# Kernel optimization log

Hardware: AMD Instinct MI355X
Metric: run time of the kernel (lower is better)

Reference implementation:

```python
import jax, jax.numpy as jnp
import numpy as np

NUM_HEADS = 16
HEAD_DIM = 128
WINDOW = 512
ROPE_BASE = 10000.0


def _rope_cos_sin(seq_len):
    inv_freq = 1.0 / (ROPE_BASE ** (jnp.arange(0, HEAD_DIM, 2, dtype=jnp.float32) / HEAD_DIM))
    freqs = jnp.arange(seq_len, dtype=jnp.float32)[:, None] * inv_freq[None, :]  # (s, d/2)
    return jnp.cos(freqs), jnp.sin(freqs)


def _apply_rotary(x, cos, sin):
    # x: (b, h, s, d); cos/sin: (s, d/2). Interleaved pairs as in the torch impl.
    x1, x2 = x[..., ::2], x[..., 1::2]
    c = cos[None, None]
    s = sin[None, None]
    r1 = x1 * c - x2 * s
    r2 = x1 * s + x2 * c
    return jnp.stack([r1, r2], axis=-1).reshape(x.shape)


def setup_inputs() -> dict:
    key = jax.random.key(0)
    ks = jax.random.split(key, 5)
    dim = NUM_HEADS * HEAD_DIM
    x = jax.random.normal(ks[0], (1, 4096, dim), dtype=jnp.float32)
    std = 0.02
    Wq = jax.random.normal(ks[1], (dim, dim), dtype=jnp.float32) * std
    Wk = jax.random.normal(ks[2], (dim, dim), dtype=jnp.float32) * std
    Wv = jax.random.normal(ks[3], (dim, dim), dtype=jnp.float32) * std
    Wo = jax.random.normal(ks[4], (dim, dim), dtype=jnp.float32) * std
    return {"x": x, "Wq": Wq, "Wk": Wk, "Wv": Wv, "Wo": Wo}


def reference(x, Wq, Wk, Wv, Wo):
    b, s, dim = x.shape
    scale = HEAD_DIM ** -0.5

    def split_heads(t):
        return t.reshape(b, s, NUM_HEADS, HEAD_DIM).transpose(0, 2, 1, 3)  # b h s d

    q = split_heads(x @ Wq.T)
    k = split_heads(x @ Wk.T)
    v = split_heads(x @ Wv.T)

    cos, sin = _rope_cos_sin(s)
    q = _apply_rotary(q, cos, sin)
    k = _apply_rotary(k, cos, sin)

    scores = jnp.einsum('bhqd,bhkd->bhqk', q, k) * scale  # (b, h, s, s)
    pos = jnp.arange(s)
    i, j = pos[:, None], pos[None, :]
    mask = (j <= i) & (i - j < WINDOW)  # sliding-window causal
    scores = jnp.where(mask[None, None], scores, -jnp.inf)
    attn = jax.nn.softmax(scores, axis=-1)

    out = jnp.einsum('bhqk,bhkd->bhqd', attn, v)
    out = out.transpose(0, 2, 1, 3).reshape(b, s, dim)
    return out @ Wo.T
```

## Files before the change

### kernel.cpp

```cpp
#include <hip/hip_runtime.h>
#include <hip/hip_bf16.h>
#include <math.h>

#define DIM 2048
#define NH 16
#define HD 128
#define WIN 512

typedef __hip_bfloat16 bf16;
using frag8 = __attribute__((ext_vector_type(8))) short;
using facc4 = __attribute__((ext_vector_type(4))) float;

__device__ inline float toF(const bf16 v) { return __bfloat162float(v); }
template <typename T> __device__ inline T fromF(float v);
template <> __device__ inline float fromF<float>(float v) { return v; }
template <> __device__ inline bf16 fromF<bf16>(float v) { return __float2bfloat16(v); }

__device__ inline unsigned bfb(float x) {
    unsigned u = __float_as_uint(x);
    u += 0x7fffu + ((u >> 16) & 1u);
    return u >> 16;
}

__device__ inline uint4 pack8(const float* p) {
    const float4 v0 = *(const float4*)p;
    const float4 v1 = *(const float4*)(p + 4);
    uint4 r;
    r.x = bfb(v0.x) | (bfb(v0.y) << 16);
    r.y = bfb(v0.z) | (bfb(v0.w) << 16);
    r.z = bfb(v1.x) | (bfb(v1.y) << 16);
    r.w = bfb(v1.z) | (bfb(v1.w) << 16);
    return r;
}

__global__ __launch_bounds__(256) void cvt_f32_bf16(const float* __restrict__ src,
                                                    bf16* __restrict__ dst, int n8) {
    const int i = blockIdx.x * 256 + threadIdx.x;
    if (i < n8) ((uint4*)dst)[i] = pack8(src + (size_t)i * 8);
}

__device__ inline void gload_lds16(const bf16* g, short* l) {
    __builtin_amdgcn_global_load_lds(
        (const __attribute__((address_space(1))) unsigned int*)g,
        (__attribute__((address_space(3))) unsigned int*)l, 16, 0, 0);
}


#define WAIT_LGKM0()                                             \
    do {                                                         \
        asm volatile("s_waitcnt lgkmcnt(0)" ::: "memory");       \
        __builtin_amdgcn_sched_barrier(0);                       \
    } while (0)

#define READ_A(BUF, MI)                                                          \
    do {                                                                         \
        _Pragma("unroll") for (int ii = 0; ii < 4; ++ii)                         \
        _Pragma("unroll") for (int kk = 0; kk < 2; ++kk) {                       \
            const int row_ = wm * 128 + (MI) * 64 + ii * 16 + mr;                \
            const int slot_ = ((kk << 2) + q) ^ (row_ & 7);                      \
            a[ii][kk] = *(const frag8*)&lds[BUF][0][row_][slot_ << 3];           \
        }                                                                        \
    } while (0)

#define READ_B(BUF, NI)                                                          \
    do {                                                                         \
        _Pragma("unroll") for (int jj = 0; jj < 2; ++jj)                         \
        _Pragma("unroll") for (int kk = 0; kk < 2; ++kk) {                       \
            const int row_ = wn * 64 + (NI) * 32 + jj * 16 + mr;                 \
            const int slot_ = ((kk << 2) + q) ^ (row_ & 7);                      \
            b[NI][jj][kk] = *(const frag8*)&lds[BUF][1][row_][slot_ << 3];       \
        }                                                                        \
    } while (0)

#define MFMA_QUAD(MI, NI)                                                        \
    do {                                                                         \
        __builtin_amdgcn_s_setprio(1);                                           \
        _Pragma("unroll") for (int ii = 0; ii < 4; ++ii)                         \
        _Pragma("unroll") for (int jj = 0; jj < 2; ++jj)                         \
        _Pragma("unroll") for (int kk = 0; kk < 2; ++kk)                         \
            acc[(MI) * 4 + ii][(NI) * 2 + jj] =                                  \
                __builtin_amdgcn_mfma_f32_16x16x32_bf16(                         \
                    a[ii][kk], b[NI][jj][kk], acc[(MI) * 4 + ii][(NI) * 2 + jj], \
                    0, 0, 0);                                                    \
        __builtin_amdgcn_s_setprio(0);                                           \
    } while (0)

template <typename TC, bool SPLIT>
__global__ __launch_bounds__(512, 2) void gemm256_8ph(const bf16* __restrict__ A,
                                                      const bf16* __restrict__ B,
                                                      TC* __restrict__ C,
                                                      bf16* __restrict__ Qp,
                                                      bf16* __restrict__ Kp,
                                                      bf16* __restrict__ Vp,
                                                      int M, int N, int K) {
    __shared__ __align__(16) short lds[2][2][256][64];
    const int tid = threadIdx.x;
    const int lane = tid & 63;
    const int w = tid >> 6;

    const int gx = gridDim.x;
    const int nwg = gx * (int)gridDim.y;
    const int lin0 = (int)blockIdx.y * gx + (int)blockIdx.x;
    const int lin = ((nwg & 7) == 0) ? (lin0 & 7) * (nwg >> 3) + (lin0 >> 3) : lin0;
    const int n0 = (lin % gx) * 256;
    const int m0 = (lin / gx) * 256;

    const int wm = w >> 2, wn = w & 3;
    const int q = lane >> 4, mr = lane & 15;
    const int sl = lane & 7, rlo = lane >> 3;
    const int rbA = wm * 128 + wn * 16;
    const int rbB = (w >> 1) * 64 + (w & 1) * 16;

    const int nt = K >> 6;
    const int nIter = nt >> 1;

    facc4 acc[8][4];
#pragma unroll
    for (int i = 0; i < 8; ++i)
#pragma unroll
        for (int j = 0; j < 4; ++j)
#pragma unroll
            for (int r = 0; r < 4; ++r) acc[i][j][r] = 0.f;

    frag8 a[4][2], b[2][2][2];

    auto stage = [&](const bf16* __restrict__ G, int grb, int mat, int buf, int ub, int t) {
        const int kt = t < nt ? t : nt - 1;
        const int k0 = kt << 6;
#pragma unroll
        for (int u = 0; u < 2; ++u) {
            const int row0 = ub + u * 8;
            const int row = row0 + rlo;
            gload_lds16(G + (size_t)(grb + row) * K + k0 + ((sl ^ rlo) << 3),
                        (short*)&lds[buf][mat][row0][0]);
        }
    };

    stage(A, m0, 0, 0, rbA, 0);
    stage(A, m0, 0, 0, rbA + 64, 0);
    stage(B, n0, 1, 0, rbB, 0);
    stage(B, n0, 1, 0, rbB + 32, 0);
    stage(A, m0, 0, 1, rbA, 1);
    stage(B, n0, 1, 1, rbB, 1);
    stage(B, n0, 1, 1, rbB + 32, 1);
    asm volatile("s_waitcnt vmcnt(6)" ::: "memory");
    __builtin_amdgcn_s_barrier();

    for (int it = 0; it < nIter; ++it) {
        const int t2 = 2 * it + 2;
        READ_A(0, 0);
        READ_B(0, 0);
        stage(A, m0, 0, 1, rbA + 64, 2 * it + 1);
        __builtin_amdgcn_s_barrier();
        WAIT_LGKM0();
        MFMA_QUAD(0, 0);
        __builtin_amdgcn_s_barrier();
        READ_B(0, 1);
        stage(A, m0, 0, 0, rbA, t2);
        __builtin_amdgcn_s_barrier();
        WAIT_LGKM0();
        MFMA_QUAD(0, 1);
        __builtin_amdgcn_s_barrier();
        READ_A(0, 1);
        stage(B, n0, 1, 0, rbB, t2);
        __builtin_amdgcn_s_barrier();
        WAIT_LGKM0();
        MFMA_QUAD(1, 0);
        __builtin_amdgcn_s_barrier();
        stage(B, n0, 1, 0, rbB + 32, t2);
        __builtin_amdgcn_s_barrier();
        __builtin_amdgcn_sched_barrier(0);
        MFMA_QUAD(1, 1);
        asm volatile("s_waitcnt vmcnt(6)" ::: "memory");
        __builtin_amdgcn_s_barrier();
        READ_A(1, 0);
        READ_B(1, 0);
        stage(A, m0, 0, 0, rbA + 64, t2);
        __builtin_amdgcn_s_barrier();
        WAIT_LGKM0();
        MFMA_QUAD(0, 0);
        __builtin_amdgcn_s_barrier();
        READ_B(1, 1);
        stage(A, m0, 0, 1, rbA, t2 + 1);
        __builtin_amdgcn_s_barrier();
        WAIT_LGKM0();
        MFMA_QUAD(0, 1);
        __builtin_amdgcn_s_barrier();
        READ_A(1, 1);
        stage(B, n0, 1, 1, rbB, t2 + 1);
        __builtin_amdgcn_s_barrier();
        WAIT_LGKM0();
        MFMA_QUAD(1, 0);
        __builtin_amdgcn_s_barrier();
        stage(B, n0, 1, 1, rbB + 32, t2 + 1);
        __builtin_amdgcn_s_barrier();
        __builtin_amdgcn_sched_barrier(0);
        MFMA_QUAD(1, 1);
        asm volatile("s_waitcnt vmcnt(6)" ::: "memory");
        __builtin_amdgcn_s_barrier();
    }

    if (SPLIT) {
        bf16* dst = (n0 < DIM) ? Qp : ((n0 < 2 * DIM) ? Kp : Vp);
        const int nb = n0 % DIM;
#pragma unroll
        for (int im = 0; im < 8; ++im)
#pragma unroll
            for (int jn = 0; jn < 4; ++jn) {
                const int col = nb + wn * 64 + jn * 16 + mr;
#pragma unroll
                for (int r = 0; r < 4; ++r) {
                    const int row = m0 + wm * 128 + im * 16 + q * 4 + r;
                    dst[(size_t)row * DIM + col] = fromF<bf16>(acc[im][jn][r]);
                }
            }
    } else {
#pragma unroll
        for (int im = 0; im < 8; ++im)
#pragma unroll
            for (int jn = 0; jn < 4; ++jn) {
                const int col = n0 + wn * 64 + jn * 16 + mr;
#pragma unroll
                for (int r = 0; r < 4; ++r) {
                    const int row = m0 + wm * 128 + im * 16 + q * 4 + r;
                    C[(size_t)row * N + col] = fromF<TC>(acc[im][jn][r]);
                }
            }
    }
}

template <typename TC>
__global__ __launch_bounds__(256) void gemm_bt_async(const bf16* __restrict__ A,
                                                     const bf16* __restrict__ B,
                                                     TC* __restrict__ C,
                                                     int M, int N, int K) {
    __shared__ short As[128 * 32];
    __shared__ short Bs[128 * 32];
    const int tid = threadIdx.x;
    const int lane = tid & 63;
    const int w = tid >> 6;
    const int m0 = blockIdx.y * 128;
    const int n0 = blockIdx.x * 128;
    const int wm = (w >> 1) * 64;
    const int wn = (w & 1) * 64;
    const int q = lane >> 4;
    const int mr = lane & 15;

    facc4 acc[4][4];
#pragma unroll
    for (int i = 0; i < 4; ++i)
#pragma unroll
        for (int j = 0; j < 4; ++j)
#pragma unroll
            for (int r = 0; r < 4; ++r) acc[i][j][r] = 0.f;

    for (int k0 = 0; k0 < K; k0 += 32) {
        __syncthreads();
#pragma unroll
        for (int u = 0; u < 2; ++u) {
            const int c = w * 128 + u * 64 + lane;
            const int row = c >> 2, col = (c & 3) * 8;
            gload_lds16(A + (size_t)(m0 + row) * K + k0 + col, As + (w * 128 + u * 64) * 8);
            gload_lds16(B + (size_t)(n0 + row) * K + k0 + col, Bs + (w * 128 + u * 64) * 8);
        }
        __syncthreads();

        frag8 af[4], bfr[4];
#pragma unroll
        for (int i = 0; i < 4; ++i)
            af[i] = *(const frag8*)&As[(wm + 16 * i + mr) * 32 + q * 8];
#pragma unroll
        for (int j = 0; j < 4; ++j)
            bfr[j] = *(const frag8*)&Bs[(wn + 16 * j + mr) * 32 + q * 8];
#pragma unroll
        for (int i = 0; i < 4; ++i)
#pragma unroll
            for (int j = 0; j < 4; ++j)
                acc[i][j] = __builtin_amdgcn_mfma_f32_16x16x32_bf16(af[i], bfr[j], acc[i][j], 0, 0, 0);
    }

#pragma unroll
    for (int i = 0; i < 4; ++i)
#pragma unroll
        for (int j = 0; j < 4; ++j) {
            const int col = n0 + wn + 16 * j + mr;
#pragma unroll
            for (int r = 0; r < 4; ++r) {
                const int row = m0 + wm + 16 * i + q * 4 + r;
                C[(size_t)row * N + col] = fromF<TC>(acc[i][j][r]);
            }
        }
}

__device__ inline uint rot_pair(uint wp, float c, float s) {
    const float x1 = __uint_as_float((wp & 0xFFFFu) << 16);
    const float x2 = __uint_as_float(wp & 0xFFFF0000u);
    const float r1 = x1 * c - x2 * s;
    const float r2 = x1 * s + x2 * c;
    return bfb(r1) | (bfb(r2) << 16);
}

__global__ __launch_bounds__(256) void rope_qk_vec(bf16* __restrict__ Q,
                                                   bf16* __restrict__ K, int S) {
    const int p = blockIdx.x * 256 + threadIdx.x;
    const int per_row = DIM / 8;
    const int s = p / per_row;
    const int off = (p % per_row) * 8;
    const int f0 = (off & 127) >> 1;
    float cs[4], sn[4];
#pragma unroll
    for (int t = 0; t < 4; ++t) {
        const float inv = __expf(-0.14391157f * (float)(f0 + t));
        sincosf((float)s * inv, &sn[t], &cs[t]);
    }
    const size_t base = (size_t)s * DIM + off;
    uint4 qv = *(uint4*)(Q + base);
    qv.x = rot_pair(qv.x, cs[0], sn[0]);
    qv.y = rot_pair(qv.y, cs[1], sn[1]);
    qv.z = rot_pair(qv.z, cs[2], sn[2]);
    qv.w = rot_pair(qv.w, cs[3], sn[3]);
    *(uint4*)(Q + base) = qv;
    uint4 kv = *(uint4*)(K + base);
    kv.x = rot_pair(kv.x, cs[0], sn[0]);
    kv.y = rot_pair(kv.y, cs[1], sn[1]);
    kv.z = rot_pair(kv.z, cs[2], sn[2]);
    kv.w = rot_pair(kv.w, cs[3], sn[3]);
    *(uint4*)(K + base) = kv;
}

__global__ __launch_bounds__(256) void transp_v(const bf16* __restrict__ V,
                                                bf16* __restrict__ Vt, int S) {
    const int tid = threadIdx.x;
    const int lane = tid & 63;
    const int w = tid >> 6;
    const int k0 = blockIdx.x * 64;
    const int h = blockIdx.y;
#pragma unroll
    for (int it = 0; it < 2; ++it) {
        const int kp = lane & 31;
        const int dc = (lane >> 5) + 2 * it + 4 * w;
        const int d0 = dc * 8;
        const bf16* vp = V + (size_t)(k0 + 2 * kp) * DIM + h * HD + d0;
        const uint4 a = *(const uint4*)vp;
        const uint4 b = *(const uint4*)(vp + DIM);
        const uint aw[4] = {a.x, a.y, a.z, a.w};
        const uint bw[4] = {b.x, b.y, b.z, b.w};
#pragma unroll
        for (int e = 0; e < 8; ++e) {
            const uint lo = (aw[e >> 1] >> (16 * (e & 1))) & 0xFFFFu;
            const uint hi = (bw[e >> 1] >> (16 * (e & 1))) & 0xFFFFu;
            ((uint*)Vt)[((((size_t)h * HD + d0 + e) * S + k0) >> 1) + kp] = lo | (hi << 16);
        }
    }
}

__global__ __launch_bounds__(256, 3) void flash_swa(const bf16* __restrict__ Q,
                                                    const bf16* __restrict__ K,
                                                    const bf16* __restrict__ Vt,
                                                    bf16* __restrict__ O, int S) {
    __shared__ __align__(16) char lds[53248];
    short* Qs = (short*)lds;
    short* Ps = (short*)lds;
    short* Ks = (short*)(lds + 17408);
    short* VtL = (short*)(lds + 34816);

    const int tid = threadIdx.x;
    const int lane = tid & 63;
    const int w = tid >> 6;
    const int q = lane >> 4;
    const int mr = lane & 15;
    const int i0 = blockIdx.x * 64;
    const int h = blockIdx.y;
    const float scale = 0.08838834764831845f;

#pragma unroll
    for (int u = 0; u < 4; ++u) {
        const int c = tid + 256 * u;
        const int row = c >> 4, col = (c & 15) * 8;
        *(uint4*)&Qs[row * 136 + col] =
            *(const uint4*)(Q + (size_t)(i0 + row) * DIM + h * HD + col);
    }
    __syncthreads();
    frag8 qf[4];
#pragma unroll
    for (int kk = 0; kk < 4; ++kk)
        qf[kk] = *(const frag8*)&Qs[(w * 16 + mr) * 136 + kk * 32 + q * 8];

    float mrow[4], lrow[4];
    facc4 oacc[8];
#pragma unroll
    for (int r = 0; r < 4; ++r) { mrow[r] = -1e30f; lrow[r] = 0.f; }
#pragma unroll
    for (int dt = 0; dt < 8; ++dt)
#pragma unroll
        for (int r = 0; r < 4; ++r) oacc[dt][r] = 0.f;

    const bf16* vtg = Vt + (size_t)h * HD * S;

    const int t0 = (i0 >= WIN) ? 0 : (WIN - i0) / 64;
    for (int t = t0; t < 9; ++t) {
        const int jb = i0 - WIN + t * 64;
        __syncthreads();

#pragma unroll
        for (int u = 0; u < 4; ++u) {
            const int c = tid + 256 * u;
            const int row = c >> 4, col = (c & 15) * 8;
            *(uint4*)&Ks[row * 136 + col] =
                *(const uint4*)(K + (size_t)(jb + row) * DIM + h * HD + col);
        }
#pragma unroll
        for (int u = 0; u < 4; ++u) {
            const int c = tid + 256 * u;
            const int d = c >> 3, k0c = (c & 7) * 8;
            *(uint4*)&VtL[d * 72 + k0c] = *(const uint4*)(vtg + (size_t)d * S + jb + k0c);
        }
        __syncthreads();

        facc4 sacc[4];
#pragma unroll
        for (int nt = 0; nt < 4; ++nt) {
#pragma unroll
            for (int r = 0; r < 4; ++r) sacc[nt][r] = 0.f;
#pragma unroll
            for (int kk = 0; kk < 4; ++kk) {
                const frag8 kfr = *(const frag8*)&Ks[(nt * 16 + mr) * 136 + kk * 32 + q * 8];
                sacc[nt] = __builtin_amdgcn_mfma_f32_16x16x32_bf16(qf[kk], kfr, sacc[nt], 0, 0, 0);
            }
        }

        float sv[4][4];
        float rmax[4] = {-1e30f, -1e30f, -1e30f, -1e30f};
#pragma unroll
        for (int nt = 0; nt < 4; ++nt) {
            const int j = jb + nt * 16 + mr;
#pragma unroll
            for (int r = 0; r < 4; ++r) {
                const int i = i0 + w * 16 + q * 4 + r;
                const bool valid = (j <= i) && (i - j < WIN);
                sv[nt][r] = valid ? sacc[nt][r] * scale : -1e30f;
                rmax[r] = fmaxf(rmax[r], sv[nt][r]);
            }
        }
#pragma unroll
        for (int msk = 1; msk <= 8; msk <<= 1)
#pragma unroll
            for (int r = 0; r < 4; ++r)
                rmax[r] = fmaxf(rmax[r], __shfl_xor(rmax[r], msk, 64));

        float alpha[4], rsum[4];
#pragma unroll
        for (int r = 0; r < 4; ++r) {
            const float mn = fmaxf(mrow[r], rmax[r]);
            alpha[r] = __expf(mrow[r] - mn);
            mrow[r] = mn;
            rsum[r] = 0.f;
        }
#pragma unroll
        for (int nt = 0; nt < 4; ++nt)
#pragma unroll
            for (int r = 0; r < 4; ++r) {
                const float pv = (sv[nt][r] > -1e29f) ? __expf(sv[nt][r] - mrow[r]) : 0.f;
                rsum[r] += pv;
                Ps[(w * 16 + q * 4 + r) * 72 + nt * 16 + mr] = (short)bfb(pv);
            }
#pragma unroll
        for (int msk = 1; msk <= 8; msk <<= 1)
#pragma unroll
            for (int r = 0; r < 4; ++r)
                rsum[r] += __shfl_xor(rsum[r], msk, 64);
#pragma unroll
        for (int r = 0; r < 4; ++r) lrow[r] = lrow[r] * alpha[r] + rsum[r];
#pragma unroll
        for (int dt = 0; dt < 8; ++dt)
#pragma unroll
            for (int r = 0; r < 4; ++r) oacc[dt][r] *= alpha[r];

        __syncthreads();

#pragma unroll
        for (int ks = 0; ks < 2; ++ks) {
            const frag8 pf = *(const frag8*)&Ps[(w * 16 + mr) * 72 + ks * 32 + q * 8];
#pragma unroll
            for (int dt = 0; dt < 8; ++dt) {
                const frag8 vf = *(const frag8*)&VtL[(dt * 16 + mr) * 72 + ks * 32 + q * 8];
                oacc[dt] = __builtin_amdgcn_mfma_f32_16x16x32_bf16(pf, vf, oacc[dt], 0, 0, 0);
            }
        }
    }

    float inv[4];
#pragma unroll
    for (int r = 0; r < 4; ++r) inv[r] = 1.0f / lrow[r];
#pragma unroll
    for (int dt = 0; dt < 8; ++dt)
#pragma unroll
        for (int r = 0; r < 4; ++r) {
            const int row = i0 + w * 16 + q * 4 + r;
            O[(size_t)row * DIM + h * HD + dt * 16 + mr] = fromF<bf16>(oacc[dt][r] * inv[r]);
        }
}

extern "C" void kernel_launch(void* const* d_in, const int* in_sizes, int n_in,
                              void* d_out, int out_size, void* d_ws, size_t ws_size,
                              hipStream_t stream) {
    const float* x  = (const float*)d_in[0];
    const float* Wq = (const float*)d_in[1];
    const float* Wk = (const float*)d_in[2];
    const float* Wv = (const float*)d_in[3];
    const float* Wo = (const float*)d_in[4];
    float* out = (float*)d_out;

    const int S = in_sizes[0] / DIM;
    const size_t elems = (size_t)S * DIM;
    const size_t wsz = (size_t)DIM * DIM;

    bf16* Q    = (bf16*)d_ws;
    bf16* K    = Q + elems;
    bf16* V    = K + elems;
    bf16* Aat  = V + elems;
    bf16* xb   = Aat + elems;
    bf16* Wcat = xb + elems;
    bf16* Wob  = Wcat + 3 * wsz;
    bf16* Vt   = xb;

    cvt_f32_bf16<<<(int)(elems / 8 / 256), 256, 0, stream>>>(x, xb, (int)(elems / 8));
    cvt_f32_bf16<<<(int)(wsz / 8 / 256), 256, 0, stream>>>(Wq, Wcat, (int)(wsz / 8));
    cvt_f32_bf16<<<(int)(wsz / 8 / 256), 256, 0, stream>>>(Wk, Wcat + wsz, (int)(wsz / 8));
    cvt_f32_bf16<<<(int)(wsz / 8 / 256), 256, 0, stream>>>(Wv, Wcat + 2 * wsz, (int)(wsz / 8));
    cvt_f32_bf16<<<(int)(wsz / 8 / 256), 256, 0, stream>>>(Wo, Wob, (int)(wsz / 8));

    gemm256_8ph<bf16, true><<<dim3(3 * DIM / 256, S / 256), 512, 0, stream>>>(
        xb, Wcat, (bf16*)nullptr, Q, K, V, S, 3 * DIM, DIM);

    rope_qk_vec<<<(int)(elems / 8 / 256), 256, 0, stream>>>(Q, K, S);

    transp_v<<<dim3(S / 64, NH), 256, 0, stream>>>(V, Vt, S);

    flash_swa<<<dim3(S / 64, NH), 256, 0, stream>>>(Q, K, Vt, Aat, S);

    gemm_bt_async<float><<<dim3(DIM / 128, S / 128), 256, 0, stream>>>(
        Aat, Wob, out, S, DIM, DIM);
}
```

Measured before the change: 389.8 us.

## Fuse RoPE and V transpose into QKV GEMM epilogue, merge weight conversions

The QKV GEMM epilogue now applies rotary embedding to Q and K in registers, using a lane shuffle to fetch each interleaved partner. It also writes V directly in transposed (head-dim major) layout, which removes the separate rope and transpose kernels and their global memory round trips. The four weight conversion launches are merged into one kernel. In exchange, sincos is now computed per output element inside the GEMM epilogue, and the transposed V stores are strided rather than contiguous, which can cost store efficiency.

```diff
diff --git a/kernel.cpp b/kernel.cpp
--- a/kernel.cpp
+++ b/kernel.cpp
@@ -37,6 +37,19 @@
                                                     bf16* __restrict__ dst, int n8) {
     const int i = blockIdx.x * 256 + threadIdx.x;
     if (i < n8) ((uint4*)dst)[i] = pack8(src + (size_t)i * 8);
+}
+
+#define W8LOG 19
+__global__ __launch_bounds__(256) void cvt4_f32_bf16(const float* __restrict__ s0,
+                                                     const float* __restrict__ s1,
+                                                     const float* __restrict__ s2,
+                                                     const float* __restrict__ s3,
+                                                     bf16* __restrict__ dst) {
+    const int i = blockIdx.x * 256 + threadIdx.x;
+    const int seg = i >> W8LOG;
+    const int off = i & ((1 << W8LOG) - 1);
+    const float* s = (seg == 0) ? s0 : (seg == 1) ? s1 : (seg == 2) ? s2 : s3;
+    ((uint4*)dst)[i] = pack8(s + (size_t)off * 8);
 }
 
 __device__ inline void gload_lds16(const bf16* g, short* l) {
@@ -201,19 +214,43 @@
     }
 
     if (SPLIT) {
-        bf16* dst = (n0 < DIM) ? Qp : ((n0 < 2 * DIM) ? Kp : Vp);
-        const int nb = n0 % DIM;
-#pragma unroll
-        for (int im = 0; im < 8; ++im)
-#pragma unroll
-            for (int jn = 0; jn < 4; ++jn) {
-                const int col = nb + wn * 64 + jn * 16 + mr;
-#pragma unroll
-                for (int r = 0; r < 4; ++r) {
-                    const int row = m0 + wm * 128 + im * 16 + q * 4 + r;
-                    dst[(size_t)row * DIM + col] = fromF<bf16>(acc[im][jn][r]);
+        if (n0 < 2 * DIM) {
+            bf16* dst = (n0 < DIM) ? Qp : Kp;
+            const int nb = n0 % DIM;
+#pragma unroll
+            for (int im = 0; im < 8; ++im) {
+                const int row = m0 + wm * 128 + im * 16 + q * 4;
+#pragma unroll
+                for (int jn = 0; jn < 4; ++jn) {
+                    const int col = nb + wn * 64 + jn * 16 + mr;
+                    const int f = (col & 127) >> 1;
+                    const float inv = __expf(-0.14391157f * (float)f);
+                    const float sgn = (col & 1) ? 1.f : -1.f;
+#pragma unroll
+                    for (int r = 0; r < 4; ++r) {
+                        const float v = acc[im][jn][r];
+                        const float p = __shfl_xor(v, 1, 64);
+                        float sn_, cs_;
+                        sincosf((float)(row + r) * inv, &sn_, &cs_);
+                        dst[(size_t)(row + r) * DIM + col] =
+                            fromF<bf16>(v * cs_ + sgn * p * sn_);
+                    }
                 }
             }
+        } else {
+#pragma unroll
+            for (int im = 0; im < 8; ++im) {
+                const int s0r = m0 + wm * 128 + im * 16 + q * 4;
+#pragma unroll
+                for (int jn = 0; jn < 4; ++jn) {
+                    const int col = (n0 - 2 * DIM) + wn * 64 + jn * 16 + mr;
+                    uint2 pk;
+                    pk.x = bfb(acc[im][jn][0]) | (bfb(acc[im][jn][1]) << 16);
+                    pk.y = bfb(acc[im][jn][2]) | (bfb(acc[im][jn][3]) << 16);
+                    *(uint2*)(Vp + (size_t)col * M + s0r) = pk;
+                }
+            }
+        }
     } else {
 #pragma unroll
         for (int im = 0; im < 8; ++im)
@@ -292,68 +329,6 @@
         }
 }
 
-__device__ inline uint rot_pair(uint wp, float c, float s) {
-    const float x1 = __uint_as_float((wp & 0xFFFFu) << 16);
-    const float x2 = __uint_as_float(wp & 0xFFFF0000u);
-    const float r1 = x1 * c - x2 * s;
-    const float r2 = x1 * s + x2 * c;
-    return bfb(r1) | (bfb(r2) << 16);
-}
-
-__global__ __launch_bounds__(256) void rope_qk_vec(bf16* __restrict__ Q,
-                                                   bf16* __restrict__ K, int S) {
-    const int p = blockIdx.x * 256 + threadIdx.x;
-    const int per_row = DIM / 8;
-    const int s = p / per_row;
-    const int off = (p % per_row) * 8;
-    const int f0 = (off & 127) >> 1;
-    float cs[4], sn[4];
-#pragma unroll
-    for (int t = 0; t < 4; ++t) {
-        const float inv = __expf(-0.14391157f * (float)(f0 + t));
-        sincosf((float)s * inv, &sn[t], &cs[t]);
-    }
-    const size_t base = (size_t)s * DIM + off;
-    uint4 qv = *(uint4*)(Q + base);
-    qv.x = rot_pair(qv.x, cs[0], sn[0]);
-    qv.y = rot_pair(qv.y, cs[1], sn[1]);
-    qv.z = rot_pair(qv.z, cs[2], sn[2]);
-    qv.w = rot_pair(qv.w, cs[3], sn[3]);
-    *(uint4*)(Q + base) = qv;
-    uint4 kv = *(uint4*)(K + base);
-    kv.x = rot_pair(kv.x, cs[0], sn[0]);
-    kv.y = rot_pair(kv.y, cs[1], sn[1]);
-    kv.z = rot_pair(kv.z, cs[2], sn[2]);
-    kv.w = rot_pair(kv.w, cs[3], sn[3]);
-    *(uint4*)(K + base) = kv;
-}
-
-__global__ __launch_bounds__(256) void transp_v(const bf16* __restrict__ V,
-                                                bf16* __restrict__ Vt, int S) {
-    const int tid = threadIdx.x;
-    const int lane = tid & 63;
-    const int w = tid >> 6;
-    const int k0 = blockIdx.x * 64;
-    const int h = blockIdx.y;
-#pragma unroll
-    for (int it = 0; it < 2; ++it) {
-        const int kp = lane & 31;
-        const int dc = (lane >> 5) + 2 * it + 4 * w;
-        const int d0 = dc * 8;
-        const bf16* vp = V + (size_t)(k0 + 2 * kp) * DIM + h * HD + d0;
-        const uint4 a = *(const uint4*)vp;
-        const uint4 b = *(const uint4*)(vp + DIM);
-        const uint aw[4] = {a.x, a.y, a.z, a.w};
-        const uint bw[4] = {b.x, b.y, b.z, b.w};
-#pragma unroll
-        for (int e = 0; e < 8; ++e) {
-            const uint lo = (aw[e >> 1] >> (16 * (e & 1))) & 0xFFFFu;
-            const uint hi = (bw[e >> 1] >> (16 * (e & 1))) & 0xFFFFu;
-            ((uint*)Vt)[((((size_t)h * HD + d0 + e) * S + k0) >> 1) + kp] = lo | (hi << 16);
-        }
-    }
-}
-
 __global__ __launch_bounds__(256, 3) void flash_swa(const bf16* __restrict__ Q,
                                                     const bf16* __restrict__ K,
                                                     const bf16* __restrict__ Vt,
@@ -522,22 +497,14 @@
     bf16* xb   = Aat + elems;
     bf16* Wcat = xb + elems;
     bf16* Wob  = Wcat + 3 * wsz;
-    bf16* Vt   = xb;
 
     cvt_f32_bf16<<<(int)(elems / 8 / 256), 256, 0, stream>>>(x, xb, (int)(elems / 8));
-    cvt_f32_bf16<<<(int)(wsz / 8 / 256), 256, 0, stream>>>(Wq, Wcat, (int)(wsz / 8));
-    cvt_f32_bf16<<<(int)(wsz / 8 / 256), 256, 0, stream>>>(Wk, Wcat + wsz, (int)(wsz / 8));
-    cvt_f32_bf16<<<(int)(wsz / 8 / 256), 256, 0, stream>>>(Wv, Wcat + 2 * wsz, (int)(wsz / 8));
-    cvt_f32_bf16<<<(int)(wsz / 8 / 256), 256, 0, stream>>>(Wo, Wob, (int)(wsz / 8));
+    cvt4_f32_bf16<<<(int)(4 * wsz / 8 / 256), 256, 0, stream>>>(Wq, Wk, Wv, Wo, Wcat);
 
     gemm256_8ph<bf16, true><<<dim3(3 * DIM / 256, S / 256), 512, 0, stream>>>(
         xb, Wcat, (bf16*)nullptr, Q, K, V, S, 3 * DIM, DIM);
 
-    rope_qk_vec<<<(int)(elems / 8 / 256), 256, 0, stream>>>(Q, K, S);
-
-    transp_v<<<dim3(S / 64, NH), 256, 0, stream>>>(V, Vt, S);
-
-    flash_swa<<<dim3(S / 64, NH), 256, 0, stream>>>(Q, K, Vt, Aat, S);
+    flash_swa<<<dim3(S / 64, NH), 256, 0, stream>>>(Q, K, V, Aat, S);
 
     gemm_bt_async<float><<<dim3(DIM / 128, S / 128), 256, 0, stream>>>(
         Aat, Wob, out, S, DIM, DIM);
```

Result: slower. 422.7 us (+8.4%).
